# Kernel tuning notes

Hardware: AMD Instinct MI355X
Metric: run time of the kernel (lower is better)

Reference implementation:

```python
import jax, jax.numpy as jnp
import numpy as np

N = 50000
E = 800000
IN_CH = 128
OUT_CH = 64


def gcn_conv(x, edge_index, W, b, n_nodes):
    """PyG GCNConv: add self-loops, symmetric deg^-1/2 normalization,
    linear transform, gather-scatter aggregation, bias."""
    src = jnp.concatenate([edge_index[0], jnp.arange(n_nodes)])
    dst = jnp.concatenate([edge_index[1], jnp.arange(n_nodes)])
    deg = jax.ops.segment_sum(jnp.ones_like(src, dtype=x.dtype), dst,
                              num_segments=n_nodes)
    dinv = jnp.where(deg > 0, jax.lax.rsqrt(deg), 0.0)
    norm = dinv[src] * dinv[dst]              # [E+N]
    h = x @ W                                  # [N, out]
    msg = h[src] * norm[:, None]               # gather + scale
    out = jax.ops.segment_sum(msg, dst, num_segments=n_nodes)  # scatter-add
    return out + b


def setup_inputs() -> dict:
    key = jax.random.key(0)
    ks = jax.random.split(key, 16)
    x = jax.random.normal(ks[0], (N, IN_CH), dtype=jnp.float32)
    edge_index = jax.random.randint(ks[1], (2, E), 0, N)

    def lin(k, fan_in, fan_out):
        kw, kb = jax.random.split(k)
        bound = 1.0 / np.sqrt(fan_in)
        W = jax.random.uniform(kw, (fan_in, fan_out), minval=-bound, maxval=bound)
        b = jax.random.uniform(kb, (fan_out,), minval=-bound, maxval=bound)
        return W, b

    # Encoder: GCN(128->128), GCN(128->64), Linear(64->64)
    eW1, eb1 = lin(ks[2], IN_CH, 2 * OUT_CH)
    eW2, eb2 = lin(ks[3], 2 * OUT_CH, OUT_CH)
    eWf, ebf = lin(ks[4], OUT_CH, OUT_CH)
    # Decoder: GCN(64->256), GCN(256->128), Linear(128->1024)
    dW1, db1 = lin(ks[5], OUT_CH, 2 * IN_CH)
    dW2, db2 = lin(ks[6], 2 * IN_CH, IN_CH)
    dWf, dbf = lin(ks[7], IN_CH, 1024)
    return {"x": x, "edge_index": edge_index,
            "eW1": eW1, "eb1": eb1, "eW2": eW2, "eb2": eb2,
            "eWf": eWf, "ebf": ebf,
            "dW1": dW1, "db1": db1, "dW2": dW2, "db2": db2,
            "dWf": dWf, "dbf": dbf}


def reference(x, edge_index, eW1, eb1, eW2, eb2, eWf, ebf,
              dW1, db1, dW2, db2, dWf, dbf):
    n = x.shape[0]
    # Encoder
    h = jax.nn.relu(gcn_conv(x, edge_index, eW1, eb1, n))
    h = gcn_conv(h, edge_index, eW2, eb2, n)
    z = h @ eWf + ebf
    # Decoder
    h = jax.nn.relu(gcn_conv(z, edge_index, dW1, db1, n))
    h = gcn_conv(h, edge_index, dW2, db2, n)
    x_hat = h @ dWf + dbf                      # [N, 1024]
    return x_hat
```

## Files before the change

### kernel.cpp

```cpp
#include <hip/hip_runtime.h>
#include <math.h>

#define NNODES 50000
#define NEDGES 800000

typedef float v4f __attribute__((ext_vector_type(4)));
typedef short bf16x8 __attribute__((ext_vector_type(8)));
typedef float f32x4 __attribute__((ext_vector_type(4)));
typedef unsigned short u16x4 __attribute__((ext_vector_type(4)));

__device__ __forceinline__ unsigned short f2bf(float f) {
    unsigned u = __float_as_uint(f);
    return (unsigned short)((u + 0x7fff + ((u >> 16) & 1)) >> 16);
}
__device__ __forceinline__ float bf2f(unsigned short h) {
    return __uint_as_float(((unsigned)h) << 16);
}


__global__ void k_init_cnt(int* __restrict__ cnt) {
    int i = blockIdx.x * 256 + threadIdx.x;
    if (i < NNODES) cnt[i] = 0;
}

__global__ void k_count(const int* __restrict__ dst, int* __restrict__ cnt) {
    int e = blockIdx.x * 256 + threadIdx.x;
    if (e < NEDGES) atomicAdd(&cnt[dst[e]], 1);
}

__global__ void k_dinv(const int* __restrict__ cnt, float* __restrict__ dinv) {
    int i = blockIdx.x * 256 + threadIdx.x;
    if (i < NNODES) dinv[i] = 1.0f / sqrtf((float)cnt[i] + 1.0f);
}


__global__ __launch_bounds__(256) void k_bsum(const int* __restrict__ cnt,
                                              int* __restrict__ bsum) {
    __shared__ int red[256];
    int i = blockIdx.x * 256 + threadIdx.x;
    int t = threadIdx.x;
    red[t] = (i < NNODES) ? cnt[i] : 0;
    __syncthreads();
#pragma unroll
    for (int off = 128; off > 0; off >>= 1) {
        if (t < off) red[t] += red[t + off];
        __syncthreads();
    }
    if (t == 0) bsum[blockIdx.x] = red[0];
}

__global__ __launch_bounds__(256) void k_bscan(int* __restrict__ bsum, int nblk) {
    __shared__ int s[256];
    int t = threadIdx.x;
    int v = (t < nblk) ? bsum[t] : 0;
    s[t] = v;
    __syncthreads();
#pragma unroll
    for (int off = 1; off < 256; off <<= 1) {
        int u = 0;
        if (t >= off) u = s[t - off];
        __syncthreads();
        if (t >= off) s[t] += u;
        __syncthreads();
    }
    if (t < nblk) bsum[t] = s[t] - v;
}

__global__ __launch_bounds__(256) void k_rowptr(int* __restrict__ cnt,
                                                const int* __restrict__ bsum,
                                                int* __restrict__ rowptr) {
    __shared__ int s[256];
    int i = blockIdx.x * 256 + threadIdx.x;
    int t = threadIdx.x;
    int v = (i < NNODES) ? cnt[i] : 0;
    s[t] = v;
    __syncthreads();
#pragma unroll
    for (int off = 1; off < 256; off <<= 1) {
        int u = 0;
        if (t >= off) u = s[t - off];
        __syncthreads();
        if (t >= off) s[t] += u;
        __syncthreads();
    }
    if (i < NNODES) {
        rowptr[i] = bsum[blockIdx.x] + s[t] - v;
        cnt[i] = 0;
    }
    if (i == 0) rowptr[NNODES] = NEDGES;
}

__global__ void k_fill(const int* __restrict__ src, const int* __restrict__ dst,
                       const int* __restrict__ rowptr, int* __restrict__ cursor,
                       const float* __restrict__ dinv,
                       int* __restrict__ col, float* __restrict__ val) {
    int e = blockIdx.x * 256 + threadIdx.x;
    if (e < NEDGES) {
        int s = src[e], d = dst[e];
        int pos = rowptr[d] + atomicAdd(&cursor[d], 1);
        col[pos] = s;
        val[pos] = dinv[s] * dinv[d];
    }
}


__global__ void k_wsplit(const float* __restrict__ W, unsigned short* __restrict__ Wh,
                         unsigned short* __restrict__ Wl, int K, int N) {
    int idx = blockIdx.x * 256 + threadIdx.x;
    if (idx >= K * N) return;
    int k = idx / N;
    int n = idx - k * N;
    float a = W[idx];
    unsigned short h = f2bf(a);
    unsigned short l = f2bf(a - bf2f(h));
    int kt = k >> 5, kr = k & 31;
    int g = kr >> 3, j = kr & 7;
    int nt = n >> 4, nc = n & 15;
    int lane = g * 16 + nc;
    size_t off = ((size_t)(kt * (N >> 4) + nt) * 64 + lane) * 8 + j;
    Wh[off] = h;
    Wl[off] = l;
}


template<int BM, int BN, int BK, int TM, int TN, bool NT, bool RELU>
__global__ __launch_bounds__(256) void k_gemm(const float* __restrict__ A,
                                              const float* __restrict__ W,
                                              const float* __restrict__ bias,
                                              float* __restrict__ C,
                                              int M, int Ncols, int K, int NB) {
    __shared__ __align__(16) float As[BK][BM];
    __shared__ __align__(16) float Ws[BK][BN];

    constexpr int CHN = TN / 4;
    constexpr int SN  = BN / CHN;
    constexpr int NTX = SN / 4;

    const int tid = threadIdx.x;
    const int tx = tid % NTX;
    const int ty = tid / NTX;
    const int bid = blockIdx.x;
    const int m0 = (bid / NB) * BM;
    const int n0 = (bid % NB) * BN;

    float acc[TM][TN];
#pragma unroll
    for (int i = 0; i < TM; ++i)
#pragma unroll
        for (int j = 0; j < TN; ++j) acc[i][j] = 0.0f;

    constexpr int AITER = (BM * BK / 4) / 256;
    constexpr int WITER = (BK * BN / 4) / 256;

    for (int k0 = 0; k0 < K; k0 += BK) {
#pragma unroll
        for (int it = 0; it < AITER; ++it) {
            int f4 = tid + it * 256;
            int row = f4 / (BK / 4);
            int kk = (f4 % (BK / 4)) * 4;
            float4 v = make_float4(0.f, 0.f, 0.f, 0.f);
            int gr = m0 + row;
            if (gr < M) v = *(const float4*)&A[(size_t)gr * K + k0 + kk];
            As[kk + 0][row] = v.x;
            As[kk + 1][row] = v.y;
            As[kk + 2][row] = v.z;
            As[kk + 3][row] = v.w;
        }
#pragma unroll
        for (int it = 0; it < WITER; ++it) {
            int f4 = tid + it * 256;
            int kk = f4 / (BN / 4);
            int nn = (f4 % (BN / 4)) * 4;
            *(float4*)&Ws[kk][nn] = *(const float4*)&W[(size_t)(k0 + kk) * Ncols + n0 + nn];
        }
        __syncthreads();

#pragma unroll
        for (int kk = 0; kk < BK; ++kk) {
            float a[TM], b[TN];
#pragma unroll
            for (int i = 0; i < TM; i += 4)
                *(float4*)&a[i] = *(const float4*)&As[kk][ty * TM + i];
#pragma unroll
            for (int c = 0; c < CHN; ++c)
                *(float4*)&b[c * 4] = *(const float4*)&Ws[kk][c * SN + tx * 4];
#pragma unroll
            for (int i = 0; i < TM; ++i)
#pragma unroll
                for (int j = 0; j < TN; ++j)
                    acc[i][j] = fmaf(a[i], b[j], acc[i][j]);
        }
        __syncthreads();
    }

#pragma unroll
    for (int i = 0; i < TM; ++i) {
        int gr = m0 + ty * TM + i;
        if (gr < M) {
#pragma unroll
            for (int c = 0; c < CHN; ++c) {
                int nb = n0 + c * SN + tx * 4;
                float4 v;
                v.x = acc[i][c * 4 + 0];
                v.y = acc[i][c * 4 + 1];
                v.z = acc[i][c * 4 + 2];
                v.w = acc[i][c * 4 + 3];
                if (bias != nullptr) {
                    v.x += bias[nb + 0];
                    v.y += bias[nb + 1];
                    v.z += bias[nb + 2];
                    v.w += bias[nb + 3];
                }
                if (RELU) {
                    v.x = fmaxf(v.x, 0.f);
                    v.y = fmaxf(v.y, 0.f);
                    v.z = fmaxf(v.z, 0.f);
                    v.w = fmaxf(v.w, 0.f);
                }
                if (NT) {
                    v4f nv;
                    nv.x = v.x; nv.y = v.y; nv.z = v.z; nv.w = v.w;
                    __builtin_nontemporal_store(nv, (v4f*)&C[(size_t)gr * Ncols + nb]);
                } else {
                    *(float4*)&C[(size_t)gr * Ncols + nb] = v;
                }
            }
        }
    }
}


template<int K, bool RELU, bool SPLIT, bool NT>
__global__ __launch_bounds__(256) void k_mfma(
        const unsigned short* __restrict__ Ah, const unsigned short* __restrict__ Al,
        const unsigned short* __restrict__ Wh, const unsigned short* __restrict__ Wl,
        const float* __restrict__ bias, float* __restrict__ C,
        unsigned short* __restrict__ Ch, unsigned short* __restrict__ Cl,
        int M, int Ncols) {
    constexpr int KT = K / 32;
    const int lane = threadIdx.x & 63;
    const int wave = threadIdx.x >> 6;
    const int wr = wave >> 1, wc = wave & 1;
    const int l15 = lane & 15, l4 = lane >> 4;
    const int bid = blockIdx.x;
    const int MBLK = (M + 127) >> 7;
    const int m0 = (bid % MBLK) * 128;
    const int n0 = (bid / MBLK) * 128;
    const int NT16 = Ncols >> 4;

    f32x4 acc[4][4];
#pragma unroll
    for (int i = 0; i < 4; ++i)
#pragma unroll
        for (int j = 0; j < 4; ++j) {
            f32x4 z = {0.f, 0.f, 0.f, 0.f};
            acc[i][j] = z;
        }

    int arow[4];
#pragma unroll
    for (int mf = 0; mf < 4; ++mf) {
        int r = m0 + wr * 64 + mf * 16 + l15;
        arow[mf] = r < M ? r : M - 1;
    }
    const int ntbase = (n0 + wc * 64) >> 4;

#pragma unroll
    for (int kt = 0; kt < KT; ++kt) {
        bf16x8 ah[4], al[4], bh[4], bl[4];
        const int ka = kt * 32 + l4 * 8;
#pragma unroll
        for (int mf = 0; mf < 4; ++mf) {
            ah[mf] = *(const bf16x8*)&Ah[(size_t)arow[mf] * K + ka];
            al[mf] = *(const bf16x8*)&Al[(size_t)arow[mf] * K + ka];
        }
#pragma unroll
        for (int nf = 0; nf < 4; ++nf) {
            size_t off = ((size_t)(kt * NT16 + ntbase + nf) * 64 + lane) * 8;
            bh[nf] = *(const bf16x8*)&Wh[off];
            bl[nf] = *(const bf16x8*)&Wl[off];
        }
#pragma unroll
        for (int mf = 0; mf < 4; ++mf)
#pragma unroll
            for (int nf = 0; nf < 4; ++nf) {
                acc[mf][nf] = __builtin_amdgcn_mfma_f32_16x16x32_bf16(ah[mf], bh[nf], acc[mf][nf], 0, 0, 0);
                acc[mf][nf] = __builtin_amdgcn_mfma_f32_16x16x32_bf16(ah[mf], bl[nf], acc[mf][nf], 0, 0, 0);
                acc[mf][nf] = __builtin_amdgcn_mfma_f32_16x16x32_bf16(al[mf], bh[nf], acc[mf][nf], 0, 0, 0);
            }
    }

    float bv[4];
#pragma unroll
    for (int nf = 0; nf < 4; ++nf)
        bv[nf] = bias ? bias[n0 + wc * 64 + nf * 16 + l15] : 0.0f;

#pragma unroll
    for (int mf = 0; mf < 4; ++mf) {
        int gr0 = m0 + wr * 64 + mf * 16 + l4 * 4;
#pragma unroll
        for (int r = 0; r < 4; ++r) {
            int gr = gr0 + r;
            if (gr < M) {
#pragma unroll
                for (int nf = 0; nf < 4; ++nf) {
                    float v = acc[mf][nf][r] + bv[nf];
                    if (RELU) v = fmaxf(v, 0.f);
                    size_t ci = (size_t)gr * Ncols + n0 + wc * 64 + nf * 16 + l15;
                    if (SPLIT) {
                        unsigned short h = f2bf(v);
                        Ch[ci] = h;
                        Cl[ci] = f2bf(v - bf2f(h));
                    } else if (NT) {
                        __builtin_nontemporal_store(v, &C[ci]);
                    } else {
                        C[ci] = v;
                    }
                }
            }
        }
    }
}


template<int CH, bool RELU, bool HB, bool SPLIT>
__global__ __launch_bounds__(256) void k_spmm(const float* __restrict__ H,
                                              const float* __restrict__ dinv,
                                              const int* __restrict__ rowptr,
                                              const int* __restrict__ col,
                                              const float* __restrict__ val,
                                              const float* __restrict__ bias,
                                              float* __restrict__ out,
                                              unsigned short* __restrict__ Oh,
                                              unsigned short* __restrict__ Ol) {
    constexpr int CV = CH / 4;
    int t = blockIdx.x * 256 + threadIdx.x;
    int row = t / CV;
    if (row >= NNODES) return;
    int c = (t % CV) * 4;

    float dv = dinv[row];
    float s2 = dv * dv;
    float4 h = *(const float4*)&H[(size_t)row * CH + c];
    float ax, ay, az, aw;
    if (HB) {
        float4 b = *(const float4*)&bias[c];
        ax = fmaf(h.x, s2, b.x);
        ay = fmaf(h.y, s2, b.y);
        az = fmaf(h.z, s2, b.z);
        aw = fmaf(h.w, s2, b.w);
    } else {
        ax = h.x * s2;
        ay = h.y * s2;
        az = h.z * s2;
        aw = h.w * s2;
    }

    const int e0 = rowptr[row], e1 = rowptr[row + 1];
    int e = e0;
    for (; e + 8 <= e1; e += 8) {
        int s[8];
        float w[8];
#pragma unroll
        for (int u = 0; u < 8; ++u) { s[u] = col[e + u]; w[u] = val[e + u]; }
        float4 hv[8];
#pragma unroll
        for (int u = 0; u < 8; ++u)
            hv[u] = *(const float4*)&H[(size_t)s[u] * CH + c];
#pragma unroll
        for (int u = 0; u < 8; ++u) {
            ax = fmaf(hv[u].x, w[u], ax);
            ay = fmaf(hv[u].y, w[u], ay);
            az = fmaf(hv[u].z, w[u], az);
            aw = fmaf(hv[u].w, w[u], aw);
        }
    }
    for (; e < e1; ++e) {
        int sidx = col[e];
        float w = val[e];
        float4 hv = *(const float4*)&H[(size_t)sidx * CH + c];
        ax = fmaf(hv.x, w, ax);
        ay = fmaf(hv.y, w, ay);
        az = fmaf(hv.z, w, az);
        aw = fmaf(hv.w, w, aw);
    }
    if (RELU) {
        ax = fmaxf(ax, 0.f);
        ay = fmaxf(ay, 0.f);
        az = fmaxf(az, 0.f);
        aw = fmaxf(aw, 0.f);
    }
    if (SPLIT) {
        u16x4 hvv, lvv;
        hvv.x = f2bf(ax); lvv.x = f2bf(ax - bf2f(hvv.x));
        hvv.y = f2bf(ay); lvv.y = f2bf(ay - bf2f(hvv.y));
        hvv.z = f2bf(az); lvv.z = f2bf(az - bf2f(hvv.z));
        hvv.w = f2bf(aw); lvv.w = f2bf(aw - bf2f(hvv.w));
        *(u16x4*)&Oh[(size_t)row * CH + c] = hvv;
        *(u16x4*)&Ol[(size_t)row * CH + c] = lvv;
    } else {
        float4 o;
        o.x = ax; o.y = ay; o.z = az; o.w = aw;
        *(float4*)&out[(size_t)row * CH + c] = o;
    }
}


extern "C" void kernel_launch(void* const* d_in, const int* in_sizes, int n_in,
                              void* d_out, int out_size, void* d_ws, size_t ws_size,
                              hipStream_t stream) {
    const float* x   = (const float*)d_in[0];
    const int*   ei  = (const int*)d_in[1];
    const float* eW1 = (const float*)d_in[2];
    const float* eb1 = (const float*)d_in[3];
    const float* eW2 = (const float*)d_in[4];
    const float* eb2 = (const float*)d_in[5];
    const float* eWf = (const float*)d_in[6];
    const float* ebf = (const float*)d_in[7];
    const float* dW1 = (const float*)d_in[8];
    const float* db1 = (const float*)d_in[9];
    const float* dW2 = (const float*)d_in[10];
    const float* db2 = (const float*)d_in[11];
    const float* dWf = (const float*)d_in[12];
    const float* dbf = (const float*)d_in[13];
    float* out = (float*)d_out;

    char* ws = (char*)d_ws;
    size_t off = 0;
    auto alloc = [&](size_t bytes) { size_t r = off; off += (bytes + 255) & ~(size_t)255; return r; };
    float* dinv   = (float*)(ws + alloc((size_t)NNODES * 4));
    int*   cnt    = (int*)  (ws + alloc((size_t)NNODES * 4));
    int*   rowptr = (int*)  (ws + alloc((size_t)(NNODES + 1) * 4));
    int*   bsum   = (int*)  (ws + alloc((size_t)256 * 4));
    int*   col    = (int*)  (ws + alloc((size_t)NEDGES * 4));
    float* val    = (float*)(ws + alloc((size_t)NEDGES * 4));
    float* B1     = (float*)(ws + alloc((size_t)NNODES * 256 * 4));
    unsigned short* Wfh = (unsigned short*)(ws + alloc((size_t)128 * 1024 * 2));
    unsigned short* Wfl = (unsigned short*)(ws + alloc((size_t)128 * 1024 * 2));
    unsigned short* W1h = (unsigned short*)(ws + alloc((size_t)64 * 256 * 2));
    unsigned short* W1l = (unsigned short*)(ws + alloc((size_t)64 * 256 * 2));
    unsigned short* W2h = (unsigned short*)(ws + alloc((size_t)256 * 128 * 2));
    unsigned short* W2l = (unsigned short*)(ws + alloc((size_t)256 * 128 * 2));

    float* B2 = out;
    unsigned short* Gh  = (unsigned short*)B2;
    unsigned short* Gl  = (unsigned short*)((char*)B2 + (size_t)NNODES * 64 * 2);
    unsigned short* A3h = (unsigned short*)B1;
    unsigned short* A3l = (unsigned short*)((char*)B1 + (size_t)NNODES * 256 * 2);
    unsigned short* Ah  = (unsigned short*)B1;
    unsigned short* Al  = (unsigned short*)((char*)B1 + (size_t)NNODES * 128 * 2);

    const int* src = ei;
    const int* dst = ei + NEDGES;

    const int gN = (NNODES + 255) / 256;
    const int gE = (NEDGES + 255) / 256;

    k_init_cnt<<<gN, 256, 0, stream>>>(cnt);
    k_count<<<gE, 256, 0, stream>>>(dst, cnt);
    k_dinv<<<gN, 256, 0, stream>>>(cnt, dinv);
    k_bsum<<<gN, 256, 0, stream>>>(cnt, bsum);
    k_bscan<<<1, 256, 0, stream>>>(bsum, gN);
    k_rowptr<<<gN, 256, 0, stream>>>(cnt, bsum, rowptr);
    k_fill<<<gE, 256, 0, stream>>>(src, dst, rowptr, cnt, dinv, col, val);
    k_wsplit<<<(128 * 1024 + 255) / 256, 256, 0, stream>>>(dWf, Wfh, Wfl, 128, 1024);
    k_wsplit<<<(64 * 256 + 255) / 256, 256, 0, stream>>>(dW1, W1h, W1l, 64, 256);
    k_wsplit<<<(256 * 128 + 255) / 256, 256, 0, stream>>>(dW2, W2h, W2l, 256, 128);

    const int MB = (NNODES + 127) / 128;

    k_gemm<128,128,16,8,8,false,false><<<MB, 256, 0, stream>>>(x, eW1, nullptr, B1, NNODES, 128, 128, 1);
    k_spmm<128,true,true,false><<<(NNODES * 32 + 255) / 256, 256, 0, stream>>>(B1, dinv, rowptr, col, val, eb1, B2, nullptr, nullptr);
    k_gemm<128,64,16,8,4,false,false><<<MB, 256, 0, stream>>>(B2, eW2, nullptr, B1, NNODES, 64, 128, 1);
    k_spmm<64,false,true,false><<<(NNODES * 16 + 255) / 256, 256, 0, stream>>>(B1, dinv, rowptr, col, val, eb2, B2, nullptr, nullptr);
    k_gemm<128,64,16,8,4,false,false><<<MB, 256, 0, stream>>>(B2, eWf, ebf, B1, NNODES, 64, 64, 1);

    k_spmm<64,false,false,true><<<(NNODES * 16 + 255) / 256, 256, 0, stream>>>(B1, dinv, rowptr, col, val, nullptr, nullptr, Gh, Gl);
    k_mfma<64,true,true,false><<<MB * 2, 256, 0, stream>>>(Gh, Gl, W1h, W1l, db1, nullptr, A3h, A3l, NNODES, 256);
    k_mfma<256,false,false,false><<<MB, 256, 0, stream>>>(A3h, A3l, W2h, W2l, nullptr, B2, nullptr, nullptr, NNODES, 128);
    k_spmm<128,false,true,true><<<(NNODES * 32 + 255) / 256, 256, 0, stream>>>(B2, dinv, rowptr, col, val, db2, nullptr, Ah, Al);
    k_mfma<128,false,false,true><<<MB * 8, 256, 0, stream>>>(Ah, Al, Wfh, Wfl, dbf, out, nullptr, nullptr, NNODES, 1024);
}
```

Measured before the change: 699.6 us.

## Store GEMM outputs in 16-channel slices and gather per slice in SpMM

The GEMMs that feed aggregation now write their output in a channel-sliced layout ([CH/16][N][16]). The SpMM is rewritten as a persistent grid-stride kernel that processes one 16-channel slice at a time across 64-row blocks. The intent is to shrink the gathered working set per pass to N*64 bytes so neighbor gathers hit in cache more often. The cost is extra passes over the CSR index and value arrays, one per slice, and 64-byte-wide gathers instead of full-row ones.

```diff
diff --git a/kernel.cpp b/kernel.cpp
--- a/kernel.cpp
+++ b/kernel.cpp
@@ -123,7 +123,7 @@
 }
 
 
-template<int BM, int BN, int BK, int TM, int TN, bool NT, bool RELU>
+template<int BM, int BN, int BK, int TM, int TN, bool NT, bool RELU, bool SLICED>
 __global__ __launch_bounds__(256) void k_gemm(const float* __restrict__ A,
                                               const float* __restrict__ W,
                                               const float* __restrict__ bias,
@@ -217,12 +217,15 @@
                     v.z = fmaxf(v.z, 0.f);
                     v.w = fmaxf(v.w, 0.f);
                 }
+                float* dst = SLICED
+                    ? &C[((size_t)(nb >> 4) * M + gr) * 16 + (nb & 15)]
+                    : &C[(size_t)gr * Ncols + nb];
                 if (NT) {
                     v4f nv;
                     nv.x = v.x; nv.y = v.y; nv.z = v.z; nv.w = v.w;
-                    __builtin_nontemporal_store(nv, (v4f*)&C[(size_t)gr * Ncols + nb]);
+                    __builtin_nontemporal_store(nv, (v4f*)dst);
                 } else {
-                    *(float4*)&C[(size_t)gr * Ncols + nb] = v;
+                    *(float4*)dst = v;
                 }
             }
         }
@@ -230,7 +233,7 @@
 }
 
 
-template<int K, bool RELU, bool SPLIT, bool NT>
+template<int K, bool RELU, bool SPLIT, bool NT, bool SLICED>
 __global__ __launch_bounds__(256) void k_mfma(
         const unsigned short* __restrict__ Ah, const unsigned short* __restrict__ Al,
         const unsigned short* __restrict__ Wh, const unsigned short* __restrict__ Wl,
@@ -306,15 +309,18 @@
                 for (int nf = 0; nf < 4; ++nf) {
                     float v = acc[mf][nf][r] + bv[nf];
                     if (RELU) v = fmaxf(v, 0.f);
-                    size_t ci = (size_t)gr * Ncols + n0 + wc * 64 + nf * 16 + l15;
+                    int cn = n0 + wc * 64 + nf * 16 + l15;
                     if (SPLIT) {
+                        size_t ci = (size_t)gr * Ncols + cn;
                         unsigned short h = f2bf(v);
                         Ch[ci] = h;
                         Cl[ci] = f2bf(v - bf2f(h));
-                    } else if (NT) {
-                        __builtin_nontemporal_store(v, &C[ci]);
                     } else {
-                        C[ci] = v;
+                        size_t ci = SLICED
+                            ? (((size_t)(cn >> 4) * M + gr) * 16 + l15)
+                            : ((size_t)gr * Ncols + cn);
+                        if (NT) __builtin_nontemporal_store(v, &C[ci]);
+                        else C[ci] = v;
                     }
                 }
             }
@@ -324,84 +330,93 @@
 
 
 template<int CH, bool RELU, bool HB, bool SPLIT>
-__global__ __launch_bounds__(256) void k_spmm(const float* __restrict__ H,
-                                              const float* __restrict__ dinv,
-                                              const int* __restrict__ rowptr,
-                                              const int* __restrict__ col,
-                                              const float* __restrict__ val,
-                                              const float* __restrict__ bias,
-                                              float* __restrict__ out,
-                                              unsigned short* __restrict__ Oh,
-                                              unsigned short* __restrict__ Ol) {
-    constexpr int CV = CH / 4;
-    int t = blockIdx.x * 256 + threadIdx.x;
-    int row = t / CV;
-    if (row >= NNODES) return;
-    int c = (t % CV) * 4;
-
-    float dv = dinv[row];
-    float s2 = dv * dv;
-    float4 h = *(const float4*)&H[(size_t)row * CH + c];
-    float ax, ay, az, aw;
-    if (HB) {
-        float4 b = *(const float4*)&bias[c];
-        ax = fmaf(h.x, s2, b.x);
-        ay = fmaf(h.y, s2, b.y);
-        az = fmaf(h.z, s2, b.z);
-        aw = fmaf(h.w, s2, b.w);
-    } else {
-        ax = h.x * s2;
-        ay = h.y * s2;
-        az = h.z * s2;
-        aw = h.w * s2;
-    }
-
-    const int e0 = rowptr[row], e1 = rowptr[row + 1];
-    int e = e0;
-    for (; e + 8 <= e1; e += 8) {
-        int s[8];
-        float w[8];
-#pragma unroll
-        for (int u = 0; u < 8; ++u) { s[u] = col[e + u]; w[u] = val[e + u]; }
-        float4 hv[8];
-#pragma unroll
-        for (int u = 0; u < 8; ++u)
-            hv[u] = *(const float4*)&H[(size_t)s[u] * CH + c];
-#pragma unroll
-        for (int u = 0; u < 8; ++u) {
-            ax = fmaf(hv[u].x, w[u], ax);
-            ay = fmaf(hv[u].y, w[u], ay);
-            az = fmaf(hv[u].z, w[u], az);
-            aw = fmaf(hv[u].w, w[u], aw);
-        }
-    }
-    for (; e < e1; ++e) {
-        int sidx = col[e];
-        float w = val[e];
-        float4 hv = *(const float4*)&H[(size_t)sidx * CH + c];
-        ax = fmaf(hv.x, w, ax);
-        ay = fmaf(hv.y, w, ay);
-        az = fmaf(hv.z, w, az);
-        aw = fmaf(hv.w, w, aw);
-    }
-    if (RELU) {
-        ax = fmaxf(ax, 0.f);
-        ay = fmaxf(ay, 0.f);
-        az = fmaxf(az, 0.f);
-        aw = fmaxf(aw, 0.f);
-    }
-    if (SPLIT) {
-        u16x4 hvv, lvv;
-        hvv.x = f2bf(ax); lvv.x = f2bf(ax - bf2f(hvv.x));
-        hvv.y = f2bf(ay); lvv.y = f2bf(ay - bf2f(hvv.y));
-        hvv.z = f2bf(az); lvv.z = f2bf(az - bf2f(hvv.z));
-        hvv.w = f2bf(aw); lvv.w = f2bf(aw - bf2f(hvv.w));
-        *(u16x4*)&Oh[(size_t)row * CH + c] = hvv;
-        *(u16x4*)&Ol[(size_t)row * CH + c] = lvv;
-    } else {
-        float4 o;
-        o.x = ax; o.y = ay; o.z = az; o.w = aw;
-        *(float4*)&out[(size_t)row * CH + c] = o;
+__global__ __launch_bounds__(256) void k_spmm_s(const float* __restrict__ H,
+                                                const float* __restrict__ dinv,
+                                                const int* __restrict__ rowptr,
+                                                const int* __restrict__ col,
+                                                const float* __restrict__ val,
+                                                const float* __restrict__ bias,
+                                                float* __restrict__ out,
+                                                unsigned short* __restrict__ Oh,
+                                                unsigned short* __restrict__ Ol) {
+    constexpr int NS = CH / 16;
+    const int RB = (NNODES + 63) / 64;
+    const int NITEM = NS * RB;
+    const int rq = threadIdx.x >> 2;
+    const int c4 = (threadIdx.x & 3) * 4;
+
+    for (int item = blockIdx.x; item < NITEM; item += gridDim.x) {
+        const int s  = item / RB;
+        const int rb = item - s * RB;
+        const int row = rb * 64 + rq;
+        if (row >= NNODES) continue;
+        const float* __restrict__ Hs = H + (size_t)s * NNODES * 16;
+
+        float dv = dinv[row];
+        float s2 = dv * dv;
+        float4 h = *(const float4*)&Hs[(size_t)row * 16 + c4];
+        float ax, ay, az, aw;
+        if (HB) {
+            float4 b = *(const float4*)&bias[s * 16 + c4];
+            ax = fmaf(h.x, s2, b.x);
+            ay = fmaf(h.y, s2, b.y);
+            az = fmaf(h.z, s2, b.z);
+            aw = fmaf(h.w, s2, b.w);
+        } else {
+            ax = h.x * s2;
+            ay = h.y * s2;
+            az = h.z * s2;
+            aw = h.w * s2;
+        }
+
+        const int e0 = rowptr[row], e1 = rowptr[row + 1];
+        int e = e0;
+        for (; e + 8 <= e1; e += 8) {
+            int sx[8];
+            float w[8];
+#pragma unroll
+            for (int u = 0; u < 8; ++u) { sx[u] = col[e + u]; w[u] = val[e + u]; }
+            float4 hv[8];
+#pragma unroll
+            for (int u = 0; u < 8; ++u)
+                hv[u] = *(const float4*)&Hs[(size_t)sx[u] * 16 + c4];
+#pragma unroll
+            for (int u = 0; u < 8; ++u) {
+                ax = fmaf(hv[u].x, w[u], ax);
+                ay = fmaf(hv[u].y, w[u], ay);
+                az = fmaf(hv[u].z, w[u], az);
+                aw = fmaf(hv[u].w, w[u], aw);
+            }
+        }
+        for (; e < e1; ++e) {
+            int sidx = col[e];
+            float w = val[e];
+            float4 hv = *(const float4*)&Hs[(size_t)sidx * 16 + c4];
+            ax = fmaf(hv.x, w, ax);
+            ay = fmaf(hv.y, w, ay);
+            az = fmaf(hv.z, w, az);
+            aw = fmaf(hv.w, w, aw);
+        }
+        if (RELU) {
+            ax = fmaxf(ax, 0.f);
+            ay = fmaxf(ay, 0.f);
+            az = fmaxf(az, 0.f);
+            aw = fmaxf(aw, 0.f);
+        }
+        const int ch = s * 16 + c4;
+        if (SPLIT) {
+            u16x4 hvv, lvv;
+            hvv.x = f2bf(ax); lvv.x = f2bf(ax - bf2f(hvv.x));
+            hvv.y = f2bf(ay); lvv.y = f2bf(ay - bf2f(hvv.y));
+            hvv.z = f2bf(az); lvv.z = f2bf(az - bf2f(hvv.z));
+            hvv.w = f2bf(aw); lvv.w = f2bf(aw - bf2f(hvv.w));
+            *(u16x4*)&Oh[(size_t)row * CH + ch] = hvv;
+            *(u16x4*)&Ol[(size_t)row * CH + ch] = lvv;
+        } else {
+            float4 o;
+            o.x = ax; o.y = ay; o.z = az; o.w = aw;
+            *(float4*)&out[(size_t)row * CH + ch] = o;
+        }
     }
 }
 
@@ -468,16 +483,17 @@
     k_wsplit<<<(256 * 128 + 255) / 256, 256, 0, stream>>>(dW2, W2h, W2l, 256, 128);
 
     const int MB = (NNODES + 127) / 128;
-
-    k_gemm<128,128,16,8,8,false,false><<<MB, 256, 0, stream>>>(x, eW1, nullptr, B1, NNODES, 128, 128, 1);
-    k_spmm<128,true,true,false><<<(NNODES * 32 + 255) / 256, 256, 0, stream>>>(B1, dinv, rowptr, col, val, eb1, B2, nullptr, nullptr);
-    k_gemm<128,64,16,8,4,false,false><<<MB, 256, 0, stream>>>(B2, eW2, nullptr, B1, NNODES, 64, 128, 1);
-    k_spmm<64,false,true,false><<<(NNODES * 16 + 255) / 256, 256, 0, stream>>>(B1, dinv, rowptr, col, val, eb2, B2, nullptr, nullptr);
-    k_gemm<128,64,16,8,4,false,false><<<MB, 256, 0, stream>>>(B2, eWf, ebf, B1, NNODES, 64, 64, 1);
-
-    k_spmm<64,false,false,true><<<(NNODES * 16 + 255) / 256, 256, 0, stream>>>(B1, dinv, rowptr, col, val, nullptr, nullptr, Gh, Gl);
-    k_mfma<64,true,true,false><<<MB * 2, 256, 0, stream>>>(Gh, Gl, W1h, W1l, db1, nullptr, A3h, A3l, NNODES, 256);
-    k_mfma<256,false,false,false><<<MB, 256, 0, stream>>>(A3h, A3l, W2h, W2l, nullptr, B2, nullptr, nullptr, NNODES, 128);
-    k_spmm<128,false,true,true><<<(NNODES * 32 + 255) / 256, 256, 0, stream>>>(B2, dinv, rowptr, col, val, db2, nullptr, Ah, Al);
-    k_mfma<128,false,false,true><<<MB * 8, 256, 0, stream>>>(Ah, Al, Wfh, Wfl, dbf, out, nullptr, nullptr, NNODES, 1024);
-}
+    const int SPG = 768;
+
+    k_gemm<128,128,16,8,8,false,false,true><<<MB, 256, 0, stream>>>(x, eW1, nullptr, B1, NNODES, 128, 128, 1);
+    k_spmm_s<128,true,true,false><<<SPG, 256, 0, stream>>>(B1, dinv, rowptr, col, val, eb1, B2, nullptr, nullptr);
+    k_gemm<128,64,16,8,4,false,false,true><<<MB, 256, 0, stream>>>(B2, eW2, nullptr, B1, NNODES, 64, 128, 1);
+    k_spmm_s<64,false,true,false><<<SPG, 256, 0, stream>>>(B1, dinv, rowptr, col, val, eb2, B2, nullptr, nullptr);
+    k_gemm<128,64,16,8,4,false,false,true><<<MB, 256, 0, stream>>>(B2, eWf, ebf, B1, NNODES, 64, 64, 1);
+
+    k_spmm_s<64,false,false,true><<<SPG, 256, 0, stream>>>(B1, dinv, rowptr, col, val, nullptr, nullptr, Gh, Gl);
+    k_mfma<64,true,true,false,false><<<MB * 2, 256, 0, stream>>>(Gh, Gl, W1h, W1l, db1, nullptr, A3h, A3l, NNODES, 256);
+    k_mfma<256,false,false,false,true><<<MB, 256, 0, stream>>>(A3h, A3l, W2h, W2l, nullptr, B2, nullptr, nullptr, NNODES, 128);
+    k_spmm_s<128,false,true,true><<<SPG, 256, 0, stream>>>(B2, dinv, rowptr, col, val, db2, nullptr, Ah, Al);
+    k_mfma<128,false,false,true,false><<<MB * 8, 256, 0, stream>>>(Ah, Al, Wfh, Wfl, dbf, out, nullptr, nullptr, NNODES, 1024);
+}
```

New measurement: 761.3 us. 8.8% more time.
